# Kernel optimization log

Measured on AMD Instinct MI355X. Metric: run time of the kernel, lower is better.

The kernel has to match this reference:

```python
import jax, jax.numpy as jnp
import numpy as np

B, S, HID = 1, 2048, 4096
NH, NKV, D = 32, 8, 128          # query heads, kv heads, head_dim
GROUPS = NH // NKV               # GQA repeat factor = 4
WINDOW = 1024                    # sliding-window size
ROPE_BASE = 10000.0


def setup_inputs() -> dict:
    key = jax.random.key(0)
    k = jax.random.split(key, 5)
    hidden_states = jax.random.normal(k[0], (B, S, HID), jnp.float32)
    Wq = jax.random.normal(k[1], (HID, HID), jnp.float32) * 0.02
    Wk = jax.random.normal(k[2], (NKV * D, HID), jnp.float32) * 0.02
    Wv = jax.random.normal(k[3], (NKV * D, HID), jnp.float32) * 0.02
    Wo = jax.random.normal(k[4], (HID, HID), jnp.float32) * 0.02
    position_ids = jnp.arange(S, dtype=jnp.int64 if jax.config.jax_enable_x64 else jnp.int32)[None, :]
    # Sliding-window causal additive mask [B,1,S,S]: key j visible to query i iff i-WINDOW < j <= i
    i = jnp.arange(S)
    visible = (i[None, :] <= i[:, None]) & (i[:, None] - i[None, :] < WINDOW)
    neg = jnp.finfo(jnp.float32).min
    attention_mask = jnp.where(visible, 0.0, neg)[None, None, :, :].astype(jnp.float32)
    return {"hidden_states": hidden_states, "attention_mask": attention_mask,
            "position_ids": position_ids, "Wq": Wq, "Wk": Wk, "Wv": Wv, "Wo": Wo}


def _rotate_half(x):
    x1, x2 = x[..., : D // 2], x[..., D // 2:]
    return jnp.concatenate((-x2, x1), axis=-1)


def _rope_cos_sin(position_ids, dtype):
    # inv_freq over even dims; gather-by-position_ids == direct indexing
    inv_freq = 1.0 / (ROPE_BASE ** (jnp.arange(0, D, 2, dtype=jnp.float32) / D))  # [D/2]
    freqs = position_ids.astype(jnp.float32)[..., None] * inv_freq                # [B,S,D/2]
    emb = jnp.concatenate((freqs, freqs), axis=-1)                                # [B,S,D]
    cos = jnp.cos(emb)[:, None, :, :].astype(dtype)                               # [B,1,S,D]
    sin = jnp.sin(emb)[:, None, :, :].astype(dtype)
    return cos, sin


def reference(hidden_states, attention_mask, position_ids, Wq, Wk, Wv, Wo):
    bsz, q_len, _ = hidden_states.shape
    # projections (nn.Linear: y = x @ W.T)
    q = (hidden_states @ Wq.T).reshape(bsz, q_len, NH, D).transpose(0, 2, 1, 3)    # [B,NH,S,D]
    k = (hidden_states @ Wk.T).reshape(bsz, q_len, NKV, D).transpose(0, 2, 1, 3)   # [B,NKV,S,D]
    v = (hidden_states @ Wv.T).reshape(bsz, q_len, NKV, D).transpose(0, 2, 1, 3)
    cos, sin = _rope_cos_sin(position_ids, q.dtype)
    q = q * cos + _rotate_half(q) * sin
    k = k * cos + _rotate_half(k) * sin
    # GQA repeat_kv (repeat_interleave along head dim)
    k = jnp.repeat(k, GROUPS, axis=1)                                              # [B,NH,S,D]
    v = jnp.repeat(v, GROUPS, axis=1)
    scores = jnp.einsum('bhqd,bhkd->bhqk', q, k) / np.sqrt(D)                       # [B,NH,S,S]
    scores = scores + attention_mask
    scores = jnp.maximum(scores, jnp.finfo(scores.dtype).min)
    probs = jax.nn.softmax(scores.astype(jnp.float32), axis=-1).astype(q.dtype)
    out = jnp.einsum('bhqk,bhkd->bhqd', probs, v)                                   # [B,NH,S,D]
    out = out.transpose(0, 2, 1, 3).reshape(bsz, q_len, HID)
    return out @ Wo.T
```

## Files before the change

### kernel.cpp

```cpp
#include <hip/hip_runtime.h>

#define S_LEN 2048
#define HID   4096
#define NH    32
#define NKV   8
#define DH    128
#define KVD   (NKV*DH)
#define WIN   1024
#define NTOT  6144

typedef __bf16 bf16_t;
typedef __bf16 bfrag  __attribute__((ext_vector_type(8)));
typedef __bf16 bf4    __attribute__((ext_vector_type(4)));
typedef float  ffrag  __attribute__((ext_vector_type(4)));
typedef float  f4     __attribute__((ext_vector_type(4)));

__global__ __launch_bounds__(256) void f32_to_bf16_kernel(const float* __restrict__ src,
                                                          bf16_t* __restrict__ dst, int n4) {
  int i = blockIdx.x * 256 + threadIdx.x;
  if (i < n4) {
    ffrag v = *(const ffrag*)(src + (size_t)i * 4);
    bf4 o;
    o[0] = (bf16_t)v[0]; o[1] = (bf16_t)v[1]; o[2] = (bf16_t)v[2]; o[3] = (bf16_t)v[3];
    *(bf4*)(dst + (size_t)i * 4) = o;
  }
}

__global__ __launch_bounds__(256) void cvt4_kernel(const float* __restrict__ h,
    const float* __restrict__ Wq, const float* __restrict__ Wk, const float* __restrict__ Wv,
    bf16_t* __restrict__ hB, bf16_t* __restrict__ WqB,
    bf16_t* __restrict__ WkB, bf16_t* __restrict__ WvB) {
  int i = blockIdx.x * 256 + threadIdx.x;
  const int N0 = S_LEN * HID / 4;
  const int N1 = N0 + HID * HID / 4;
  const int N2 = N1 + KVD * HID / 4;
  const float* s; bf16_t* d; int off;
  if (i < N0)      { s = h;  d = hB;  off = i; }
  else if (i < N1) { s = Wq; d = WqB; off = i - N0; }
  else if (i < N2) { s = Wk; d = WkB; off = i - N1; }
  else             { s = Wv; d = WvB; off = i - N2; }
  ffrag v = *(const ffrag*)(s + (size_t)off * 4);
  bf4 o;
  o[0] = (bf16_t)v[0]; o[1] = (bf16_t)v[1]; o[2] = (bf16_t)v[2]; o[3] = (bf16_t)v[3];
  *(bf4*)(d + (size_t)off * 4) = o;
}

__device__ __forceinline__ void load_lds16(const bf16_t* g, bf16_t* l) {
  __builtin_amdgcn_global_load_lds((__attribute__((address_space(1))) void*)g,
                                   (__attribute__((address_space(3))) void*)l,
                                   16, 0, 0);
}

template <int OUT_MODE>
__device__ __forceinline__ void gemm_core(const bf16_t* __restrict__ A,
                                          const bf16_t* __restrict__ B,
                                          void* __restrict__ Cv,
                                          int row0, int brow0, int ccol0,
                                          int N, int K, int kbeg, int kend,
                                          bf16_t* As, bf16_t* Bs) {
  const int tid  = threadIdx.x;
  const int wave = tid >> 6;
  const int lane = tid & 63;
  const int wr = wave >> 1, wc = wave & 1;
  const int m  = lane & 15, qd = lane >> 4;

  ffrag acc[4][4];
#pragma unroll
  for (int i = 0; i < 4; ++i)
#pragma unroll
    for (int j = 0; j < 4; ++j) {
      acc[i][j][0] = 0.f; acc[i][j][1] = 0.f; acc[i][j][2] = 0.f; acc[i][j][3] = 0.f;
    }

  const int srow = wave * 32 + (lane >> 3);
  const int scol = (lane & 7) * 8;
  const bf16_t* Ag = A + (size_t)(row0  + srow) * K + scol;
  const bf16_t* Bg = B + (size_t)(brow0 + srow) * K + scol;

  for (int k0 = kbeg; k0 < kend; k0 += 64) {
#pragma unroll
    for (int i = 0; i < 4; ++i) {
      load_lds16(Ag + (size_t)(i * 8) * K + k0, &As[(wave * 32 + i * 8) * 64]);
      load_lds16(Bg + (size_t)(i * 8) * K + k0, &Bs[(wave * 32 + i * 8) * 64]);
    }
    __syncthreads();
#pragma unroll
    for (int ks = 0; ks < 2; ++ks) {
      bfrag av[4], bv[4];
#pragma unroll
      for (int t = 0; t < 4; ++t) {
        av[t] = *(const bfrag*)&As[(wr * 64 + t * 16 + m) * 64 + ks * 32 + qd * 8];
        bv[t] = *(const bfrag*)&Bs[(wc * 64 + t * 16 + m) * 64 + ks * 32 + qd * 8];
      }
#pragma unroll
      for (int mt = 0; mt < 4; ++mt)
#pragma unroll
        for (int nt = 0; nt < 4; ++nt)
          acc[mt][nt] = __builtin_amdgcn_mfma_f32_16x16x32_bf16(av[mt], bv[nt], acc[mt][nt], 0, 0, 0);
    }
    __syncthreads();
  }

#pragma unroll
  for (int mt = 0; mt < 4; ++mt)
#pragma unroll
    for (int nt = 0; nt < 4; ++nt)
#pragma unroll
      for (int r = 0; r < 4; ++r) {
        int row = row0 + wr * 64 + mt * 16 + qd * 4 + r;
        int col = ccol0 + wc * 64 + nt * 16 + m;
        if (OUT_MODE == 1)      ((bf16_t*)Cv)[(size_t)row * N + col] = (bf16_t)acc[mt][nt][r];
        else if (OUT_MODE == 0) ((float*)Cv)[(size_t)row * N + col]  = acc[mt][nt][r];
        else                    atomicAdd(&((float*)Cv)[(size_t)row * N + col], acc[mt][nt][r]);
      }
}

__global__ __launch_bounds__(256) void gemm_qkv_kernel(const bf16_t* __restrict__ hB,
    const bf16_t* __restrict__ WqB, const bf16_t* __restrict__ WkB, const bf16_t* __restrict__ WvB,
    bf16_t* __restrict__ Cpart) {
  __shared__ __align__(16) bf16_t As[128 * 64];
  __shared__ __align__(16) bf16_t Bs[128 * 64];
  const int bx = blockIdx.x;
  const int row0 = blockIdx.y * 128;
  const int kz = blockIdx.z;
  const bf16_t* B; int brow0;
  if (bx < 32)      { B = WqB; brow0 = bx * 128; }
  else if (bx < 40) { B = WkB; brow0 = (bx - 32) * 128; }
  else              { B = WvB; brow0 = (bx - 40) * 128; }
  bf16_t* C = Cpart + (size_t)kz * S_LEN * NTOT;
  gemm_core<1>(hB, B, C, row0, brow0, bx * 128, NTOT, HID, kz * 2048, kz * 2048 + 2048, As, Bs);
}

__global__ __launch_bounds__(256) void gemm_out_kernel(const bf16_t* __restrict__ A,
    const bf16_t* __restrict__ B, float* __restrict__ out) {
  __shared__ __align__(16) bf16_t As[128 * 64];
  __shared__ __align__(16) bf16_t Bs[128 * 64];
  const int c0 = blockIdx.x * 128;
  const int kz = blockIdx.z;
  gemm_core<2>(A, B, out, blockIdx.y * 128, c0, c0, HID, HID, kz * 2048, kz * 2048 + 2048, As, Bs);
}

__global__ __launch_bounds__(256) void ropecvt_kernel(const bf16_t* __restrict__ Cpart,
                                                      bf16_t* __restrict__ Qb,
                                                      bf16_t* __restrict__ Kb,
                                                      bf16_t* __restrict__ Vb) {
  int idx = blockIdx.x * 256 + threadIdx.x;
  int g  = idx & 7;
  int t  = idx >> 3;
  int hh = t % 48;
  int s  = t / 48;
  const bf16_t* r0 = Cpart + (size_t)s * NTOT + hh * 128;
  const bf16_t* r1 = r0 + (size_t)S_LEN * NTOT;
  bfrag a0 = *(const bfrag*)&r0[g * 8];
  bfrag a1 = *(const bfrag*)&r0[g * 8 + 64];
  bfrag b0 = *(const bfrag*)&r1[g * 8];
  bfrag b1 = *(const bfrag*)&r1[g * 8 + 64];
  bf16_t* p;
  bool rope;
  if (hh < NH)           { p = Qb + (size_t)s * HID + hh * DH;        rope = true; }
  else if (hh < NH+NKV)  { p = Kb + (size_t)s * KVD + (hh - NH) * DH; rope = true; }
  else                   { p = Vb + (size_t)s * KVD + (hh - 40) * DH; rope = false; }
  bfrag o1, o2;
#pragma unroll
  for (int j = 0; j < 8; ++j) {
    float x1 = (float)a0[j] + (float)b0[j];
    float x2 = (float)a1[j] + (float)b1[j];
    if (rope) {
      int d = g * 8 + j;
      float inv = exp2f((float)d * (-13.287712379549449f / 64.f));
      float ang = (float)s * inv;
      float sn = sinf(ang), cs = cosf(ang);
      o1[j] = (bf16_t)(x1 * cs - x2 * sn);
      o2[j] = (bf16_t)(x2 * cs + x1 * sn);
    } else {
      o1[j] = (bf16_t)x1;
      o2[j] = (bf16_t)x2;
    }
  }
  *(bfrag*)&p[g * 8]      = o1;
  *(bfrag*)&p[g * 8 + 64] = o2;
}

#define KS_STRIDE 136
#define VT_STRIDE 72
#define PS_STRIDE 72

__global__ __launch_bounds__(256, 3) void attn_kernel(const bf16_t* __restrict__ Q,
                                                      const bf16_t* __restrict__ Kc,
                                                      const bf16_t* __restrict__ Vc,
                                                      bf16_t* __restrict__ AO) {
  const int qt   = 31 - blockIdx.x;
  const int h    = blockIdx.y;
  const int kvh  = h >> 2;
  const int q0   = qt * 64;
  const int tid  = threadIdx.x;
  const int wq   = tid >> 6;
  const int lane = tid & 63;
  const int n    = lane & 15;
  const int quad = lane >> 4;
  const float scale = 0.08838834764831845f;

  __shared__ __align__(16) bf16_t Ks[64 * KS_STRIDE];
  __shared__ __align__(16) bf16_t VT[128 * VT_STRIDE];
  __shared__ __align__(16) bf16_t Ps[4][16 * PS_STRIDE];

  bfrag aq[4];
#pragma unroll
  for (int kc = 0; kc < 4; ++kc) {
    bfrag t = *(const bfrag*)&Q[(size_t)(q0 + wq * 16 + n) * HID + h * DH + kc * 32 + quad * 8];
#pragma unroll
    for (int e = 0; e < 8; ++e) t[e] = (bf16_t)((float)t[e] * scale);
    aq[kc] = t;
  }

  ffrag acc[8];
#pragma unroll
  for (int dt = 0; dt < 8; ++dt) { acc[dt][0] = 0.f; acc[dt][1] = 0.f; acc[dt][2] = 0.f; acc[dt][3] = 0.f; }
  float lrow[4] = {0.f, 0.f, 0.f, 0.f};

  const int ktlo = (q0 >= WIN) ? ((q0 - (WIN - 1)) >> 6) : 0;
  const int kthi = (q0 + 63) >> 6;

  const int kg = tid & 15;
  const int dg = tid >> 4;

  bfrag pk[4], pv[4];
  {
    const int k0 = ktlo * 64;
#pragma unroll
    for (int i = 0; i < 4; ++i) {
      int pos = i * 256 + tid;
      pk[i] = *(const bfrag*)&Kc[(size_t)(k0 + (pos >> 4)) * KVD + kvh * DH + (pos & 15) * 8];
    }
#pragma unroll
    for (int j = 0; j < 4; ++j)
      pv[j] = *(const bfrag*)&Vc[(size_t)(k0 + j * 16 + kg) * KVD + kvh * DH + dg * 8];
  }

  for (int kt = ktlo; kt <= kthi; ++kt) {
    const int k0 = kt * 64;
    __syncthreads();
#pragma unroll
    for (int i = 0; i < 4; ++i) {
      int pos = i * 256 + tid;
      *(bfrag*)&Ks[(pos >> 4) * KS_STRIDE + (pos & 15) * 8] = pk[i];
    }
#pragma unroll
    for (int i = 0; i < 8; ++i) {
      bf4 pkk;
      pkk[0] = pv[0][i]; pkk[1] = pv[1][i]; pkk[2] = pv[2][i]; pkk[3] = pv[3][i];
      *(bf4*)&VT[(dg * 8 + i) * VT_STRIDE + kg * 4] = pkk;
    }
    __syncthreads();
    if (kt < kthi) {
      const int k1 = k0 + 64;
#pragma unroll
      for (int i = 0; i < 4; ++i) {
        int pos = i * 256 + tid;
        pk[i] = *(const bfrag*)&Kc[(size_t)(k1 + (pos >> 4)) * KVD + kvh * DH + (pos & 15) * 8];
      }
#pragma unroll
      for (int j = 0; j < 4; ++j)
        pv[j] = *(const bfrag*)&Vc[(size_t)(k1 + j * 16 + kg) * KVD + kvh * DH + dg * 8];
    }

    ffrag s[4];
#pragma unroll
    for (int nt = 0; nt < 4; ++nt) { s[nt][0] = 0.f; s[nt][1] = 0.f; s[nt][2] = 0.f; s[nt][3] = 0.f; }
#pragma unroll
    for (int kc = 0; kc < 4; ++kc) {
      bfrag bk[4];
#pragma unroll
      for (int nt = 0; nt < 4; ++nt)
        bk[nt] = *(const bfrag*)&Ks[(nt * 16 + n) * KS_STRIDE + kc * 32 + quad * 8];
#pragma unroll
      for (int nt = 0; nt < 4; ++nt)
        s[nt] = __builtin_amdgcn_mfma_f32_16x16x32_bf16(aq[kc], bk[nt], s[nt], 0, 0, 0);
    }

    const bool full = (k0 + 63 <= q0) && (q0 + 63 - k0 < WIN);
    if (!full) {
#pragma unroll
      for (int nt = 0; nt < 4; ++nt)
#pragma unroll
        for (int r = 0; r < 4; ++r) {
          int q = q0 + wq * 16 + quad * 4 + r;
          int k = k0 + nt * 16 + n;
          bool vis = (k <= q) && ((q - k) < WIN);
          if (!vis) s[nt][r] = -1e30f;
        }
    }

#pragma unroll
    for (int r = 0; r < 4; ++r) {
      bf4 pkk;
      float ps0 = __expf(s[0][r]);
      float ps1 = __expf(s[1][r]);
      float ps2 = __expf(s[2][r]);
      float ps3 = __expf(s[3][r]);
      lrow[r] += (ps0 + ps1) + (ps2 + ps3);
      pkk[0] = (bf16_t)ps0; pkk[1] = (bf16_t)ps1; pkk[2] = (bf16_t)ps2; pkk[3] = (bf16_t)ps3;
      *(bf4*)&Ps[wq][(quad * 4 + r) * PS_STRIDE + n * 4] = pkk;
    }

#pragma unroll
    for (int kc = 0; kc < 2; ++kc) {
      bfrag ap = *(const bfrag*)&Ps[wq][n * PS_STRIDE + kc * 32 + quad * 8];
#pragma unroll
      for (int dt = 0; dt < 8; ++dt) {
        bfrag bv = *(const bfrag*)&VT[(dt * 16 + n) * VT_STRIDE + kc * 32 + quad * 8];
        acc[dt] = __builtin_amdgcn_mfma_f32_16x16x32_bf16(ap, bv, acc[dt], 0, 0, 0);
      }
    }
  }

#pragma unroll
  for (int off = 1; off < 16; off <<= 1)
#pragma unroll
    for (int r = 0; r < 4; ++r) lrow[r] += __shfl_xor(lrow[r], off);
  float inv[4];
#pragma unroll
  for (int r = 0; r < 4; ++r) inv[r] = 1.f / lrow[r];
#pragma unroll
  for (int dt = 0; dt < 8; ++dt)
#pragma unroll
    for (int r = 0; r < 4; ++r)
      AO[(size_t)(q0 + wq * 16 + quad * 4 + r) * HID + h * DH + dt * 16 + n] =
          (bf16_t)(acc[dt][r] * inv[r]);
}

extern "C" void kernel_launch(void* const* d_in, const int* in_sizes, int n_in,
                              void* d_out, int out_size, void* d_ws, size_t ws_size,
                              hipStream_t stream) {
  const float* h  = (const float*)d_in[0];
  const float* Wq = (const float*)d_in[3];
  const float* Wk = (const float*)d_in[4];
  const float* Wv = (const float*)d_in[5];
  const float* Wo = (const float*)d_in[6];
  float* out = (float*)d_out;

  char* ws = (char*)d_ws;
  const size_t MB = (size_t)1 << 20;
  bf16_t* hB    = (bf16_t*)(ws + 0 * MB);
  bf16_t* Qb    = (bf16_t*)(ws + 0 * MB);
  bf16_t* WqB   = (bf16_t*)(ws + 16 * MB);
  bf16_t* WkB   = (bf16_t*)(ws + 48 * MB);
  bf16_t* WvB   = (bf16_t*)(ws + 56 * MB);
  bf16_t* Cpart = (bf16_t*)(ws + 64 * MB);
  bf16_t* WoB   = (bf16_t*)(ws + 64 * MB);
  bf16_t* AOb   = (bf16_t*)(ws + 96 * MB);
  bf16_t* Kb    = (bf16_t*)(ws + 112 * MB);
  bf16_t* Vb    = (bf16_t*)(ws + 116 * MB);

  cvt4_kernel<<<(S_LEN * HID + HID * HID + 2 * KVD * HID) / 4 / 256, 256, 0, stream>>>(
      h, Wq, Wk, Wv, hB, WqB, WkB, WvB);

  gemm_qkv_kernel<<<dim3(48, 16, 2), 256, 0, stream>>>(hB, WqB, WkB, WvB, Cpart);

  ropecvt_kernel<<<(S_LEN * 48 * 8) / 256, 256, 0, stream>>>(Cpart, Qb, Kb, Vb);

  f32_to_bf16_kernel<<<(HID * HID / 4 + 255) / 256, 256, 0, stream>>>(Wo, WoB, HID * HID / 4);

  attn_kernel<<<dim3(32, NH), 256, 0, stream>>>(Qb, Kb, Vb, AOb);

  hipMemsetAsync(out, 0, (size_t)S_LEN * HID * sizeof(float), stream);

  gemm_out_kernel<<<dim3(HID / 128, S_LEN / 128, 2), 256, 0, stream>>>(AOb, WoB, out);
}
```

Baseline: 539.3 us.

## Rewrite GEMMs as 256x256-tile, 4-stage pipelined kernels with swizzled LDS

```diff
diff --git a/kernel.cpp b/kernel.cpp
--- a/kernel.cpp
+++ b/kernel.cpp
@@ -45,102 +45,139 @@
   *(bf4*)(d + (size_t)off * 4) = o;
 }
 
+#define BK 32
+
 __device__ __forceinline__ void load_lds16(const bf16_t* g, bf16_t* l) {
   __builtin_amdgcn_global_load_lds((__attribute__((address_space(1))) void*)g,
                                    (__attribute__((address_space(3))) void*)l,
                                    16, 0, 0);
 }
 
+#define BARW() asm volatile("s_barrier" ::: "memory")
+#define WAITV(n) asm volatile("s_waitcnt vmcnt(" #n ")" ::: "memory")
+
+#define STAGE_A(t, b) { const int ko_ = (t) * BK;                      \
+    load_lds16(A0 + ko_, As + (b) * 8192 +        wlds);               \
+    load_lds16(A1 + ko_, As + (b) * 8192 + 4096 + wlds); }
+#define STAGE_B(t, b) { const int ko_ = (t) * BK;                      \
+    load_lds16(B0 + ko_, Bs + (b) * 8192 +        wlds);               \
+    load_lds16(B1 + ko_, Bs + (b) * 8192 + 4096 + wlds); }
+
 template <int OUT_MODE>
-__device__ __forceinline__ void gemm_core(const bf16_t* __restrict__ A,
-                                          const bf16_t* __restrict__ B,
-                                          void* __restrict__ Cv,
-                                          int row0, int brow0, int ccol0,
-                                          int N, int K, int kbeg, int kend,
-                                          bf16_t* As, bf16_t* Bs) {
+__device__ __forceinline__ void gemm256(const bf16_t* __restrict__ A,
+                                        const bf16_t* __restrict__ B,
+                                        void* __restrict__ Cv,
+                                        int row0, int brow0, int ccol0,
+                                        int N, int K, int kbeg, int NT) {
+  __shared__ __align__(16) bf16_t lds[65536];
+  bf16_t* As = lds;
+  bf16_t* Bs = lds + 32768;
+
   const int tid  = threadIdx.x;
   const int wave = tid >> 6;
   const int lane = tid & 63;
-  const int wr = wave >> 1, wc = wave & 1;
-  const int m  = lane & 15, qd = lane >> 4;
-
-  ffrag acc[4][4];
-#pragma unroll
-  for (int i = 0; i < 4; ++i)
-#pragma unroll
-    for (int j = 0; j < 4; ++j) {
-      acc[i][j][0] = 0.f; acc[i][j][1] = 0.f; acc[i][j][2] = 0.f; acc[i][j][3] = 0.f;
-    }
-
-  const int srow = wave * 32 + (lane >> 3);
-  const int scol = (lane & 7) * 8;
-  const bf16_t* Ag = A + (size_t)(row0  + srow) * K + scol;
-  const bf16_t* Bg = B + (size_t)(brow0 + srow) * K + scol;
-
-  for (int k0 = kbeg; k0 < kend; k0 += 64) {
-#pragma unroll
-    for (int i = 0; i < 4; ++i) {
-      load_lds16(Ag + (size_t)(i * 8) * K + k0, &As[(wave * 32 + i * 8) * 64]);
-      load_lds16(Bg + (size_t)(i * 8) * K + k0, &Bs[(wave * 32 + i * 8) * 64]);
-    }
-    __syncthreads();
-#pragma unroll
-    for (int ks = 0; ks < 2; ++ks) {
-      bfrag av[4], bv[4];
-#pragma unroll
-      for (int t = 0; t < 4; ++t) {
-        av[t] = *(const bfrag*)&As[(wr * 64 + t * 16 + m) * 64 + ks * 32 + qd * 8];
-        bv[t] = *(const bfrag*)&Bs[(wc * 64 + t * 16 + m) * 64 + ks * 32 + qd * 8];
+  const int wr   = wave >> 2;
+  const int wc   = wave & 3;
+  const int n    = lane & 15;
+  const int qd   = lane >> 4;
+  const int nh   = n >> 1;
+  const int gsel = (((n & 1) << 2) | qd) ^ nh;
+
+  const int Lb0 = (tid * 16) ^ (((tid >> 3) & 7) << 4);
+  const int sr  = Lb0 >> 6;
+  const int sc  = (Lb0 & 63) >> 1;
+  const bf16_t* A0 = A + (size_t)(row0  + sr) * K + kbeg + sc;
+  const bf16_t* A1 = A0 + (size_t)128 * K;
+  const bf16_t* B0 = B + (size_t)(brow0 + sr) * K + kbeg + sc;
+  const bf16_t* B1 = B0 + (size_t)128 * K;
+  const int wlds = wave * 512;
+
+  ffrag acc[8][4];
+#pragma unroll
+  for (int mt = 0; mt < 8; ++mt)
+#pragma unroll
+    for (int nt = 0; nt < 4; ++nt) {
+      acc[mt][nt][0] = 0.f; acc[mt][nt][1] = 0.f; acc[mt][nt][2] = 0.f; acc[mt][nt][3] = 0.f;
+    }
+
+  STAGE_A(0, 0); STAGE_B(0, 0);
+  STAGE_A(1, 1); STAGE_B(1, 1);
+  STAGE_A(2, 2); STAGE_B(2, 2);
+  WAITV(8);
+  BARW();
+
+  for (int kt = 0; kt < NT; ++kt) {
+    const int b = kt & 3;
+    const bf16_t* Ab = As + b * 8192 + (wr * 64 + nh) * 64 + gsel * 8;
+    const bf16_t* Bb = Bs + b * 8192 + (wc * 32 + nh) * 64 + gsel * 8;
+    const bool pf = (kt + 3 < NT);
+    const int bp = (kt + 3) & 3;
+
+    bfrag av[4], bv[4];
+#pragma unroll
+    for (int mt = 0; mt < 4; ++mt) av[mt] = *(const bfrag*)(Ab + mt * 512);
+#pragma unroll
+    for (int nt = 0; nt < 4; ++nt) bv[nt] = *(const bfrag*)(Bb + nt * 512);
+    if (pf) STAGE_A(kt + 3, bp);
+    BARW();
+    __builtin_amdgcn_s_setprio(1);
+#pragma unroll
+    for (int mt = 0; mt < 4; ++mt)
+#pragma unroll
+      for (int nt = 0; nt < 4; ++nt)
+        acc[mt][nt] = __builtin_amdgcn_mfma_f32_16x16x32_bf16(av[mt], bv[nt], acc[mt][nt], 0, 0, 0);
+    __builtin_amdgcn_s_setprio(0);
+    BARW();
+
+#pragma unroll
+    for (int mt = 0; mt < 4; ++mt) av[mt] = *(const bfrag*)(Ab + (mt + 4) * 512);
+    if (pf) STAGE_B(kt + 3, bp);
+    BARW();
+    __builtin_amdgcn_s_setprio(1);
+#pragma unroll
+    for (int mt = 0; mt < 4; ++mt)
+#pragma unroll
+      for (int nt = 0; nt < 4; ++nt)
+        acc[mt + 4][nt] = __builtin_amdgcn_mfma_f32_16x16x32_bf16(av[mt], bv[nt], acc[mt + 4][nt], 0, 0, 0);
+    __builtin_amdgcn_s_setprio(0);
+    if (pf)                { WAITV(8); }
+    else if (kt + 2 < NT)  { WAITV(4); }
+    else                   { WAITV(0); }
+    BARW();
+  }
+
+  const int orow = row0 + wr * 128 + qd * 4;
+  const int ocol = ccol0 + wc * 64 + n;
+#pragma unroll
+  for (int mt = 0; mt < 8; ++mt)
+#pragma unroll
+    for (int nt = 0; nt < 4; ++nt)
+#pragma unroll
+      for (int r = 0; r < 4; ++r) {
+        size_t idx = (size_t)(orow + mt * 16 + r) * N + (ocol + nt * 16);
+        if (OUT_MODE == 1) ((bf16_t*)Cv)[idx] = (bf16_t)acc[mt][nt][r];
+        else               atomicAdd(&((float*)Cv)[idx], acc[mt][nt][r]);
       }
-#pragma unroll
-      for (int mt = 0; mt < 4; ++mt)
-#pragma unroll
-        for (int nt = 0; nt < 4; ++nt)
-          acc[mt][nt] = __builtin_amdgcn_mfma_f32_16x16x32_bf16(av[mt], bv[nt], acc[mt][nt], 0, 0, 0);
-    }
-    __syncthreads();
-  }
-
-#pragma unroll
-  for (int mt = 0; mt < 4; ++mt)
-#pragma unroll
-    for (int nt = 0; nt < 4; ++nt)
-#pragma unroll
-      for (int r = 0; r < 4; ++r) {
-        int row = row0 + wr * 64 + mt * 16 + qd * 4 + r;
-        int col = ccol0 + wc * 64 + nt * 16 + m;
-        if (OUT_MODE == 1)      ((bf16_t*)Cv)[(size_t)row * N + col] = (bf16_t)acc[mt][nt][r];
-        else if (OUT_MODE == 0) ((float*)Cv)[(size_t)row * N + col]  = acc[mt][nt][r];
-        else                    atomicAdd(&((float*)Cv)[(size_t)row * N + col], acc[mt][nt][r]);
-      }
-}
-
-__global__ __launch_bounds__(256) void gemm_qkv_kernel(const bf16_t* __restrict__ hB,
+}
+
+__global__ __launch_bounds__(512, 2) void gemm_qkv_kernel(const bf16_t* __restrict__ hB,
     const bf16_t* __restrict__ WqB, const bf16_t* __restrict__ WkB, const bf16_t* __restrict__ WvB,
-    bf16_t* __restrict__ Cpart) {
-  __shared__ __align__(16) bf16_t As[128 * 64];
-  __shared__ __align__(16) bf16_t Bs[128 * 64];
+    bf16_t* __restrict__ C) {
   const int bx = blockIdx.x;
-  const int row0 = blockIdx.y * 128;
-  const int kz = blockIdx.z;
   const bf16_t* B; int brow0;
-  if (bx < 32)      { B = WqB; brow0 = bx * 128; }
-  else if (bx < 40) { B = WkB; brow0 = (bx - 32) * 128; }
-  else              { B = WvB; brow0 = (bx - 40) * 128; }
-  bf16_t* C = Cpart + (size_t)kz * S_LEN * NTOT;
-  gemm_core<1>(hB, B, C, row0, brow0, bx * 128, NTOT, HID, kz * 2048, kz * 2048 + 2048, As, Bs);
-}
-
-__global__ __launch_bounds__(256) void gemm_out_kernel(const bf16_t* __restrict__ A,
+  if (bx < 16)      { B = WqB; brow0 = bx * 256; }
+  else if (bx < 20) { B = WkB; brow0 = (bx - 16) * 256; }
+  else              { B = WvB; brow0 = (bx - 20) * 256; }
+  gemm256<1>(hB, B, C, blockIdx.y * 256, brow0, bx * 256, NTOT, HID, 0, HID / BK);
+}
+
+__global__ __launch_bounds__(512, 2) void gemm_out_kernel(const bf16_t* __restrict__ A,
     const bf16_t* __restrict__ B, float* __restrict__ out) {
-  __shared__ __align__(16) bf16_t As[128 * 64];
-  __shared__ __align__(16) bf16_t Bs[128 * 64];
-  const int c0 = blockIdx.x * 128;
-  const int kz = blockIdx.z;
-  gemm_core<2>(A, B, out, blockIdx.y * 128, c0, c0, HID, HID, kz * 2048, kz * 2048 + 2048, As, Bs);
-}
-
-__global__ __launch_bounds__(256) void ropecvt_kernel(const bf16_t* __restrict__ Cpart,
+  const int c0 = blockIdx.x * 256;
+  gemm256<2>(A, B, out, blockIdx.y * 256, c0, c0, HID, HID, blockIdx.z * 2048, 2048 / BK);
+}
+
+__global__ __launch_bounds__(256) void ropecvt_kernel(const bf16_t* __restrict__ Cqkv,
                                                       bf16_t* __restrict__ Qb,
                                                       bf16_t* __restrict__ Kb,
                                                       bf16_t* __restrict__ Vb) {
@@ -149,12 +186,9 @@
   int t  = idx >> 3;
   int hh = t % 48;
   int s  = t / 48;
-  const bf16_t* r0 = Cpart + (size_t)s * NTOT + hh * 128;
-  const bf16_t* r1 = r0 + (size_t)S_LEN * NTOT;
+  const bf16_t* r0 = Cqkv + (size_t)s * NTOT + hh * 128;
   bfrag a0 = *(const bfrag*)&r0[g * 8];
   bfrag a1 = *(const bfrag*)&r0[g * 8 + 64];
-  bfrag b0 = *(const bfrag*)&r1[g * 8];
-  bfrag b1 = *(const bfrag*)&r1[g * 8 + 64];
   bf16_t* p;
   bool rope;
   if (hh < NH)           { p = Qb + (size_t)s * HID + hh * DH;        rope = true; }
@@ -163,8 +197,8 @@
   bfrag o1, o2;
 #pragma unroll
   for (int j = 0; j < 8; ++j) {
-    float x1 = (float)a0[j] + (float)b0[j];
-    float x2 = (float)a1[j] + (float)b1[j];
+    float x1 = (float)a0[j];
+    float x2 = (float)a1[j];
     if (rope) {
       int d = g * 8 + j;
       float inv = exp2f((float)d * (-13.287712379549449f / 64.f));
@@ -346,7 +380,7 @@
   bf16_t* WqB   = (bf16_t*)(ws + 16 * MB);
   bf16_t* WkB   = (bf16_t*)(ws + 48 * MB);
   bf16_t* WvB   = (bf16_t*)(ws + 56 * MB);
-  bf16_t* Cpart = (bf16_t*)(ws + 64 * MB);
+  bf16_t* Cqkv  = (bf16_t*)(ws + 64 * MB);
   bf16_t* WoB   = (bf16_t*)(ws + 64 * MB);
   bf16_t* AOb   = (bf16_t*)(ws + 96 * MB);
   bf16_t* Kb    = (bf16_t*)(ws + 112 * MB);
@@ -355,9 +389,9 @@
   cvt4_kernel<<<(S_LEN * HID + HID * HID + 2 * KVD * HID) / 4 / 256, 256, 0, stream>>>(
       h, Wq, Wk, Wv, hB, WqB, WkB, WvB);
 
-  gemm_qkv_kernel<<<dim3(48, 16, 2), 256, 0, stream>>>(hB, WqB, WkB, WvB, Cpart);
-
-  ropecvt_kernel<<<(S_LEN * 48 * 8) / 256, 256, 0, stream>>>(Cpart, Qb, Kb, Vb);
+  gemm_qkv_kernel<<<dim3(24, 8), 512, 0, stream>>>(hB, WqB, WkB, WvB, Cqkv);
+
+  ropecvt_kernel<<<(S_LEN * 48 * 8) / 256, 256, 0, stream>>>(Cqkv, Qb, Kb, Vb);
 
   f32_to_bf16_kernel<<<(HID * HID / 4 + 255) / 256, 256, 0, stream>>>(Wo, WoB, HID * HID / 4);
 
@@ -365,5 +399,5 @@
 
   hipMemsetAsync(out, 0, (size_t)S_LEN * HID * sizeof(float), stream);
 
-  gemm_out_kernel<<<dim3(HID / 128, S_LEN / 128, 2), 256, 0, stream>>>(AOb, WoB, out);
-}
+  gemm_out_kernel<<<dim3(HID / 256, S_LEN / 256, 2), 512, 0, stream>>>(AOb, WoB, out);
+}
```

New measurement: 511.5 us. 1.05x faster.

## Rewrite GEMMs with multi-stage LDS pipeline, swizzle, and no split-K

Applied to the files above, without the earlier changes.

```diff
diff --git a/kernel.cpp b/kernel.cpp
--- a/kernel.cpp
+++ b/kernel.cpp
@@ -45,102 +45,139 @@
   *(bf4*)(d + (size_t)off * 4) = o;
 }
 
+
 __device__ __forceinline__ void load_lds16(const bf16_t* g, bf16_t* l) {
   __builtin_amdgcn_global_load_lds((__attribute__((address_space(1))) void*)g,
                                    (__attribute__((address_space(3))) void*)l,
                                    16, 0, 0);
 }
 
-template <int OUT_MODE>
-__device__ __forceinline__ void gemm_core(const bf16_t* __restrict__ A,
+#define BARW() asm volatile("s_barrier" ::: "memory")
+#define WAITV(n) asm volatile("s_waitcnt vmcnt(" #n ")" ::: "memory")
+
+template <int BNR, int OUT_MODE>
+__device__ __forceinline__ void gemm_body(const bf16_t* __restrict__ A,
                                           const bf16_t* __restrict__ B,
                                           void* __restrict__ Cv,
-                                          int row0, int brow0, int ccol0,
-                                          int N, int K, int kbeg, int kend,
-                                          bf16_t* As, bf16_t* Bs) {
+                                          int N, bf16_t* lds) {
+  constexpr int K     = 4096;
+  constexpr int NT    = K / 32;
+  constexpr int NTF   = BNR / 64;
+  constexpr int WCOLS = BNR / 4;
+  constexpr int ABUFE = 4096;
+  constexpr int BBUFE = BNR * 32;
+
+  bf16_t* Asb = lds;
+  bf16_t* Bsb = lds + 4 * ABUFE;
+
+  const int raw  = blockIdx.x;
+  const int xcd  = raw & 7;
+  const int slot = raw >> 3;
+  const int bx   = xcd * 4 + (slot & 3);
+  const int by   = slot >> 2;
+  const int row0 = by * 128;
+  const int col0 = bx * BNR;
+
   const int tid  = threadIdx.x;
   const int wave = tid >> 6;
   const int lane = tid & 63;
-  const int wr = wave >> 1, wc = wave & 1;
-  const int m  = lane & 15, qd = lane >> 4;
-
-  ffrag acc[4][4];
-#pragma unroll
-  for (int i = 0; i < 4; ++i)
-#pragma unroll
-    for (int j = 0; j < 4; ++j) {
-      acc[i][j][0] = 0.f; acc[i][j][1] = 0.f; acc[i][j][2] = 0.f; acc[i][j][3] = 0.f;
-    }
-
-  const int srow = wave * 32 + (lane >> 3);
-  const int scol = (lane & 7) * 8;
-  const bf16_t* Ag = A + (size_t)(row0  + srow) * K + scol;
-  const bf16_t* Bg = B + (size_t)(brow0 + srow) * K + scol;
-
-  for (int k0 = kbeg; k0 < kend; k0 += 64) {
-#pragma unroll
-    for (int i = 0; i < 4; ++i) {
-      load_lds16(Ag + (size_t)(i * 8) * K + k0, &As[(wave * 32 + i * 8) * 64]);
-      load_lds16(Bg + (size_t)(i * 8) * K + k0, &Bs[(wave * 32 + i * 8) * 64]);
-    }
-    __syncthreads();
-#pragma unroll
-    for (int ks = 0; ks < 2; ++ks) {
-      bfrag av[4], bv[4];
-#pragma unroll
-      for (int t = 0; t < 4; ++t) {
-        av[t] = *(const bfrag*)&As[(wr * 64 + t * 16 + m) * 64 + ks * 32 + qd * 8];
-        bv[t] = *(const bfrag*)&Bs[(wc * 64 + t * 16 + m) * 64 + ks * 32 + qd * 8];
+  const int wr = wave >> 2, wc = wave & 3;
+  const int n = lane & 15, qd = lane >> 4;
+
+  const int rsub = tid >> 2;
+  const int sg   = (tid & 3) ^ (rsub & 3);
+  const bf16_t* Ag  = A + (size_t)(row0 + rsub) * K + sg * 8;
+  const bf16_t* Bg  = B + (size_t)(col0 + rsub) * K + sg * 8;
+  const bf16_t* Bg2 = B + (size_t)(col0 + 128 + rsub) * K + sg * 8;
+  const int wbase = wave * 512;
+
+  const int lsw = n * 32 + (qd ^ (n & 3)) * 8;
+
+  ffrag acc[4][NTF];
+#pragma unroll
+  for (int mt = 0; mt < 4; ++mt)
+#pragma unroll
+    for (int nt = 0; nt < NTF; ++nt) {
+      acc[mt][nt][0] = 0.f; acc[mt][nt][1] = 0.f; acc[mt][nt][2] = 0.f; acc[mt][nt][3] = 0.f;
+    }
+
+  auto STAGE = [&](int t, int b) {
+    const int ko = t * 32;
+    load_lds16(Ag + ko, Asb + b * ABUFE + wbase);
+    load_lds16(Bg + ko, Bsb + b * BBUFE + wbase);
+    if constexpr (BNR == 192) {
+      if (tid < 256) load_lds16(Bg2 + ko, Bsb + b * BBUFE + 4096 + wbase);
+    }
+  };
+
+  STAGE(0, 0); STAGE(1, 1); STAGE(2, 2);
+  if constexpr (BNR == 192) { if (wave < 4) { WAITV(6); } else { WAITV(4); } }
+  else { WAITV(4); }
+  BARW();
+
+  for (int t = 0; t < NT; ++t) {
+    const int b = t & 3;
+    if (t + 3 < NT) STAGE(t + 3, (t + 3) & 3);
+
+    const bf16_t* pa = Asb + b * ABUFE + wr * 2048 + lsw;
+    const bf16_t* pb = Bsb + b * BBUFE + wc * (WCOLS * 32) + lsw;
+    bfrag av[4], bv[NTF];
+#pragma unroll
+    for (int mt = 0; mt < 4; ++mt) av[mt] = *(const bfrag*)(pa + mt * 512);
+#pragma unroll
+    for (int nt = 0; nt < NTF; ++nt) bv[nt] = *(const bfrag*)(pb + nt * 512);
+
+    __builtin_amdgcn_s_setprio(1);
+#pragma unroll
+    for (int mt = 0; mt < 4; ++mt)
+#pragma unroll
+      for (int nt = 0; nt < NTF; ++nt)
+        acc[mt][nt] = __builtin_amdgcn_mfma_f32_16x16x32_bf16(av[mt], bv[nt], acc[mt][nt], 0, 0, 0);
+    __builtin_amdgcn_s_setprio(0);
+
+    if (t + 1 < NT) {
+      if (t + 3 < NT) {
+        if constexpr (BNR == 192) { if (wave < 4) { WAITV(6); } else { WAITV(4); } }
+        else { WAITV(4); }
+      } else if (t + 2 < NT) {
+        if constexpr (BNR == 192) { if (wave < 4) { WAITV(3); } else { WAITV(2); } }
+        else { WAITV(2); }
+      } else {
+        WAITV(0);
       }
-#pragma unroll
-      for (int mt = 0; mt < 4; ++mt)
-#pragma unroll
-        for (int nt = 0; nt < 4; ++nt)
-          acc[mt][nt] = __builtin_amdgcn_mfma_f32_16x16x32_bf16(av[mt], bv[nt], acc[mt][nt], 0, 0, 0);
-    }
-    __syncthreads();
-  }
-
+      BARW();
+    }
+  }
+
+  const int orow = row0 + wr * 64 + qd * 4;
+  const int ocol = col0 + wc * WCOLS + n;
 #pragma unroll
   for (int mt = 0; mt < 4; ++mt)
 #pragma unroll
-    for (int nt = 0; nt < 4; ++nt)
+    for (int nt = 0; nt < NTF; ++nt)
 #pragma unroll
       for (int r = 0; r < 4; ++r) {
-        int row = row0 + wr * 64 + mt * 16 + qd * 4 + r;
-        int col = ccol0 + wc * 64 + nt * 16 + m;
-        if (OUT_MODE == 1)      ((bf16_t*)Cv)[(size_t)row * N + col] = (bf16_t)acc[mt][nt][r];
-        else if (OUT_MODE == 0) ((float*)Cv)[(size_t)row * N + col]  = acc[mt][nt][r];
-        else                    atomicAdd(&((float*)Cv)[(size_t)row * N + col], acc[mt][nt][r]);
+        size_t idx = (size_t)(orow + mt * 16 + r) * N + (ocol + nt * 16);
+        if (OUT_MODE == 1) ((bf16_t*)Cv)[idx] = (bf16_t)acc[mt][nt][r];
+        else               ((float*)Cv)[idx]  = acc[mt][nt][r];
       }
 }
 
-__global__ __launch_bounds__(256) void gemm_qkv_kernel(const bf16_t* __restrict__ hB,
-    const bf16_t* __restrict__ WqB, const bf16_t* __restrict__ WkB, const bf16_t* __restrict__ WvB,
-    bf16_t* __restrict__ Cpart) {
-  __shared__ __align__(16) bf16_t As[128 * 64];
-  __shared__ __align__(16) bf16_t Bs[128 * 64];
-  const int bx = blockIdx.x;
-  const int row0 = blockIdx.y * 128;
-  const int kz = blockIdx.z;
-  const bf16_t* B; int brow0;
-  if (bx < 32)      { B = WqB; brow0 = bx * 128; }
-  else if (bx < 40) { B = WkB; brow0 = (bx - 32) * 128; }
-  else              { B = WvB; brow0 = (bx - 40) * 128; }
-  bf16_t* C = Cpart + (size_t)kz * S_LEN * NTOT;
-  gemm_core<1>(hB, B, C, row0, brow0, bx * 128, NTOT, HID, kz * 2048, kz * 2048 + 2048, As, Bs);
-}
-
-__global__ __launch_bounds__(256) void gemm_out_kernel(const bf16_t* __restrict__ A,
-    const bf16_t* __restrict__ B, float* __restrict__ out) {
-  __shared__ __align__(16) bf16_t As[128 * 64];
-  __shared__ __align__(16) bf16_t Bs[128 * 64];
-  const int c0 = blockIdx.x * 128;
-  const int kz = blockIdx.z;
-  gemm_core<2>(A, B, out, blockIdx.y * 128, c0, c0, HID, HID, kz * 2048, kz * 2048 + 2048, As, Bs);
-}
-
-__global__ __launch_bounds__(256) void ropecvt_kernel(const bf16_t* __restrict__ Cpart,
+__global__ __launch_bounds__(512, 4) void gemm_qkv_kernel(const bf16_t* __restrict__ hB,
+                                                          const bf16_t* __restrict__ Wqkv,
+                                                          bf16_t* __restrict__ C) {
+  __shared__ __align__(16) bf16_t lds[4 * 4096 + 4 * 6144];
+  gemm_body<192, 1>(hB, Wqkv, C, NTOT, lds);
+}
+
+__global__ __launch_bounds__(512, 4) void gemm_out_kernel(const bf16_t* __restrict__ A,
+                                                          const bf16_t* __restrict__ B,
+                                                          float* __restrict__ out) {
+  __shared__ __align__(16) bf16_t lds[4 * 4096 + 4 * 4096];
+  gemm_body<128, 0>(A, B, out, HID, lds);
+}
+
+__global__ __launch_bounds__(256) void ropecvt_kernel(const bf16_t* __restrict__ Cqkv,
                                                       bf16_t* __restrict__ Qb,
                                                       bf16_t* __restrict__ Kb,
                                                       bf16_t* __restrict__ Vb) {
@@ -149,12 +186,9 @@
   int t  = idx >> 3;
   int hh = t % 48;
   int s  = t / 48;
-  const bf16_t* r0 = Cpart + (size_t)s * NTOT + hh * 128;
-  const bf16_t* r1 = r0 + (size_t)S_LEN * NTOT;
+  const bf16_t* r0 = Cqkv + (size_t)s * NTOT + hh * 128;
   bfrag a0 = *(const bfrag*)&r0[g * 8];
   bfrag a1 = *(const bfrag*)&r0[g * 8 + 64];
-  bfrag b0 = *(const bfrag*)&r1[g * 8];
-  bfrag b1 = *(const bfrag*)&r1[g * 8 + 64];
   bf16_t* p;
   bool rope;
   if (hh < NH)           { p = Qb + (size_t)s * HID + hh * DH;        rope = true; }
@@ -163,8 +197,8 @@
   bfrag o1, o2;
 #pragma unroll
   for (int j = 0; j < 8; ++j) {
-    float x1 = (float)a0[j] + (float)b0[j];
-    float x2 = (float)a1[j] + (float)b1[j];
+    float x1 = (float)a0[j];
+    float x2 = (float)a1[j];
     if (rope) {
       int d = g * 8 + j;
       float inv = exp2f((float)d * (-13.287712379549449f / 64.f));
@@ -346,7 +380,7 @@
   bf16_t* WqB   = (bf16_t*)(ws + 16 * MB);
   bf16_t* WkB   = (bf16_t*)(ws + 48 * MB);
   bf16_t* WvB   = (bf16_t*)(ws + 56 * MB);
-  bf16_t* Cpart = (bf16_t*)(ws + 64 * MB);
+  bf16_t* Cqkv  = (bf16_t*)(ws + 64 * MB);
   bf16_t* WoB   = (bf16_t*)(ws + 64 * MB);
   bf16_t* AOb   = (bf16_t*)(ws + 96 * MB);
   bf16_t* Kb    = (bf16_t*)(ws + 112 * MB);
@@ -355,15 +389,13 @@
   cvt4_kernel<<<(S_LEN * HID + HID * HID + 2 * KVD * HID) / 4 / 256, 256, 0, stream>>>(
       h, Wq, Wk, Wv, hB, WqB, WkB, WvB);
 
-  gemm_qkv_kernel<<<dim3(48, 16, 2), 256, 0, stream>>>(hB, WqB, WkB, WvB, Cpart);
-
-  ropecvt_kernel<<<(S_LEN * 48 * 8) / 256, 256, 0, stream>>>(Cpart, Qb, Kb, Vb);
+  gemm_qkv_kernel<<<512, 512, 0, stream>>>(hB, WqB, Cqkv);
+
+  ropecvt_kernel<<<(S_LEN * 48 * 8) / 256, 256, 0, stream>>>(Cqkv, Qb, Kb, Vb);
 
   f32_to_bf16_kernel<<<(HID * HID / 4 + 255) / 256, 256, 0, stream>>>(Wo, WoB, HID * HID / 4);
 
   attn_kernel<<<dim3(32, NH), 256, 0, stream>>>(Qb, Kb, Vb, AOb);
 
-  hipMemsetAsync(out, 0, (size_t)S_LEN * HID * sizeof(float), stream);
-
-  gemm_out_kernel<<<dim3(HID / 128, S_LEN / 128, 2), 256, 0, stream>>>(AOb, WoB, out);
-}
+  gemm_out_kernel<<<512, 512, 0, stream>>>(AOb, WoB, out);
+}
```

After: 475.9 us. 1.13x faster.
